# Performance work log

Hardware: AMD Instinct MI355X
Metric: run time of the kernel (lower is better)

The kernel has to match this reference:

```python
import jax, jax.numpy as jnp
import numpy as np

B, N, F, L = 4, 8192, 64, 2


def setup_inputs() -> dict:
    key = jax.random.key(0)
    k1, k2, k3 = jax.random.split(key, 3)
    x = jax.random.normal(k1, (B, N, F), dtype=jnp.float32)
    net_params = jax.random.normal(k2, (L * F * F,), dtype=jnp.float32)
    A = jax.random.normal(k3, (N, N), dtype=jnp.float32)
    return {"x": x, "t": 0, "net_params": net_params, "A": A}


def reference(x, t, net_params, A):
    # weights: [L, F, F]
    weights = net_params.reshape(L, F, F)
    # x: [B, N, F] (original does x.view(-1, A.size(1), features))
    z = x.reshape(-1, A.shape[1], F)
    for i in range(L):
        # GCN_operation: Z_out = A @ Z @ W_i  (the nested vmm loops emulate exactly this)
        h = jnp.einsum('mn,bnf->bmf', A, z)          # [B, N, F]
        z = jnp.einsum('bmf,fg->bmg', h, weights[i])  # [B, N, F]
        z = jax.nn.relu(z)
    return z
```

## Files before the change

kernel.cpp:

```cpp
#include <hip/hip_runtime.h>
#include <stdint.h>


#define MK 8192

typedef float f32x4 __attribute__((ext_vector_type(4)));
typedef uint32_t u32x4 __attribute__((ext_vector_type(4)));
typedef uint32_t u32x2 __attribute__((ext_vector_type(2)));
typedef __bf16 bf16x8 __attribute__((ext_vector_type(8)));

__device__ inline uint16_t f2bf(float f) {
  uint32_t u = __builtin_bit_cast(uint32_t, f);
  u += 0x7fffu + ((u >> 16) & 1u);
  return (uint16_t)(u >> 16);
}
__device__ inline float bf2f(uint32_t lo16) {
  return __builtin_bit_cast(float, lo16 << 16);
}

#define GLD(src, dstbase)                                                                    \
  __builtin_amdgcn_global_load_lds((const __attribute__((address_space(1))) uint32_t*)(src), \
                                   (__attribute__((address_space(3))) uint32_t*)(dstbase),   \
                                   16, 0, 0)

__global__ __launch_bounds__(256) void zw0(const float* __restrict__ x,
                                           const float* __restrict__ net,
                                           uint16_t* __restrict__ Zt) {
  __shared__ float Wl[64 * 64];
  __shared__ float rows[64][65];
  const int b = blockIdx.y, n0 = blockIdx.x * 64, tid = threadIdx.x;
  for (int i = tid * 4; i < 4096; i += 1024) {
    f32x4 v = *(const f32x4*)(net + i);
    Wl[i] = v[0]; Wl[i + 1] = v[1]; Wl[i + 2] = v[2]; Wl[i + 3] = v[3];
  }
  const float* src = x + ((uint64_t)b * MK + n0) * 64;
  for (int i = tid * 4; i < 4096; i += 1024) {
    f32x4 v = *(const f32x4*)(src + i);
    int r = i >> 6, f = i & 63;
    rows[r][f] = v[0]; rows[r][f + 1] = v[1]; rows[r][f + 2] = v[2]; rows[r][f + 3] = v[3];
  }
  __syncthreads();
  const int nl = tid & 63, g0 = (tid >> 6) * 16;
  float s[16];
#pragma unroll
  for (int j = 0; j < 16; ++j) s[j] = 0.f;
  for (int f = 0; f < 64; ++f) {
    float rv = rows[nl][f];
#pragma unroll
    for (int j = 0; j < 16; ++j) s[j] = fmaf(rv, Wl[f * 64 + g0 + j], s[j]);
  }
  uint16_t* dst = Zt + (uint64_t)(b * 64 + g0) * MK + n0 + nl;
#pragma unroll
  for (int j = 0; j < 16; ++j) dst[(uint64_t)j * MK] = f2bf(s[j]);
}

__global__ __launch_bounds__(512, 2) void gemm1(const float* __restrict__ Af,
                                                const uint16_t* __restrict__ Bt,
                                                uint16_t* __restrict__ Ab,
                                                uint16_t* __restrict__ P) {
  __shared__ __align__(16) uint16_t LB[65536];
#define AS1(b) (LB + (b)*16384)
#define BS1(b) (LB + 32768 + (b)*16384)
  const int bid = (int)blockIdx.x;
  const int s = bid & 7, bm = bid >> 3;
  const int row0 = bm * 256, k0 = s * 1024;
  const int tid = threadIdx.x, wid = tid >> 6, lane = tid & 63;
  const int wr = wid >> 2, wc = wid & 3;

  const int lsub = lane >> 3;
  const int ksrc = ((lane & 7) ^ lsub) << 3;
  const uint16_t* gB0 = Bt + (uint64_t)(4 * wid * 8 + lsub) * MK + k0 + ksrc;
  const int lBo = 4 * wid * 512;

  const int arow = (8 * wid) * 4 + (lane >> 4);
  const int acol = (lane & 15) * 4;
  const float* gA0 = Af + (uint64_t)(row0 + arow) * MK + k0 + acol;
  const int koct = (lane & 15) >> 1, krem = (lane & 1) * 4;

  f32x4 acc[8][4] = {};
  f32x4 rv[8];

  auto loadA = [&](int kofs) {
#pragma unroll
    for (int j = 0; j < 8; ++j)
      rv[j] = __builtin_nontemporal_load((const f32x4*)(gA0 + (uint64_t)j * 4 * MK + kofs));
  };
  auto stageA = [&](int buf, int kofs) {
#pragma unroll
    for (int j = 0; j < 8; ++j) {
      const int r = arow + j * 4;
      u32x2 w;
      w[0] = (uint32_t)f2bf(rv[j][0]) | ((uint32_t)f2bf(rv[j][1]) << 16);
      w[1] = (uint32_t)f2bf(rv[j][2]) | ((uint32_t)f2bf(rv[j][3]) << 16);
      *(u32x2*)&AS1(buf)[r * 64 + ((koct ^ (r & 7)) << 3) + krem] = w;
      *(u32x2*)(Ab + (uint64_t)(row0 + r) * MK + k0 + kofs + acol) = w;
    }
  };

  loadA(0);
#pragma unroll
  for (int j = 0; j < 4; ++j) GLD(gB0 + (uint64_t)j * 8 * MK, &BS1(0)[lBo + j * 512]);
  stageA(0, 0);
  __syncthreads();

  int buf = 0;
  for (int t = 0; t < 16; ++t) {
    const int nxt = (t + 1) * 64;
    if (t < 15) {
      loadA(nxt);
#pragma unroll
      for (int j = 0; j < 4; ++j) GLD(gB0 + (uint64_t)j * 8 * MK + nxt, &BS1(buf ^ 1)[lBo + j * 512]);
    }
#pragma unroll
    for (int kk = 0; kk < 2; ++kk) {
      const int kb = kk * 4 + (lane >> 4);
      bf16x8 a[8], b[4];
#pragma unroll
      for (int mi = 0; mi < 8; ++mi) {
        const int r = wr * 128 + mi * 16 + (lane & 15);
        a[mi] = *(const bf16x8*)&AS1(buf)[r * 64 + ((kb ^ (r & 7)) << 3)];
      }
#pragma unroll
      for (int n = 0; n < 4; ++n) {
        const int r = wc * 64 + n * 16 + (lane & 15);
        b[n] = *(const bf16x8*)&BS1(buf)[r * 64 + ((kb ^ (r & 7)) << 3)];
      }
#pragma unroll
      for (int mi = 0; mi < 8; ++mi)
#pragma unroll
        for (int n = 0; n < 4; ++n)
          acc[mi][n] = __builtin_amdgcn_mfma_f32_16x16x32_bf16(a[mi], b[n], acc[mi][n], 0, 0, 0);
    }
    if (t < 15) stageA(buf ^ 1, nxt);
    __syncthreads();
    buf ^= 1;
  }

  __syncthreads();
  const int lr = (lane >> 4) * 4, lc = lane & 15;
#pragma unroll
  for (int mi = 0; mi < 8; ++mi)
#pragma unroll
    for (int n = 0; n < 4; ++n)
#pragma unroll
      for (int j = 0; j < 4; ++j)
        LB[(wr * 128 + mi * 16 + lr + j) * 256 + (wc * 64 + n * 16 + lc)] = f2bf(acc[mi][n][j]);
  __syncthreads();
  uint16_t* Pp = P + (uint64_t)s * 2097152 + (uint64_t)row0 * 256;
#pragma unroll
  for (int i = 0; i < 16; ++i) {
    u32x4 v = *(const u32x4*)&LB[i * 4096 + tid * 8];
    *(u32x4*)(Pp + i * 4096 + tid * 8) = v;
  }
#undef AS1
#undef BS1
}

__global__ __launch_bounds__(512, 2) void gemm2(const uint16_t* __restrict__ Ab,
                                                const uint16_t* __restrict__ Bt,
                                                uint16_t* __restrict__ P) {
  __shared__ __align__(16) uint16_t LB[65536];
#define AS2(b) (LB + (b)*16384)
#define BS2(b) (LB + 32768 + (b)*16384)
  const int bid = (int)blockIdx.x;
  const int s = bid & 7, bm = bid >> 3;
  const int row0 = bm * 256, k0 = s * 1024;
  const int tid = threadIdx.x, wid = tid >> 6, lane = tid & 63;
  const int wr = wid >> 2, wc = wid & 3;

  const int lsub = lane >> 3;
  const int ksrc = ((lane & 7) ^ lsub) << 3;
  const uint16_t* gA0 = Ab + (uint64_t)(row0 + 4 * wid * 8 + lsub) * MK + k0 + ksrc;
  const uint16_t* gB0 = Bt + (uint64_t)(4 * wid * 8 + lsub) * MK + k0 + ksrc;
  const int lo = 4 * wid * 512;

  f32x4 acc[8][4] = {};

#pragma unroll
  for (int j = 0; j < 4; ++j) {
    GLD(gA0 + (uint64_t)j * 8 * MK, &AS2(0)[lo + j * 512]);
    GLD(gB0 + (uint64_t)j * 8 * MK, &BS2(0)[lo + j * 512]);
  }

  int buf = 0;
  for (int t = 0; t < 16; ++t) {
    const int tko = ((t + 1) < 16 ? (t + 1) : 15) * 64;
#pragma unroll
    for (int j = 0; j < 4; ++j) {
      GLD(gA0 + (uint64_t)j * 8 * MK + tko, &AS2(buf ^ 1)[lo + j * 512]);
      GLD(gB0 + (uint64_t)j * 8 * MK + tko, &BS2(buf ^ 1)[lo + j * 512]);
    }
    asm volatile("s_waitcnt vmcnt(8)" ::: "memory");
    __builtin_amdgcn_s_barrier();
    __builtin_amdgcn_sched_barrier(0);

    bf16x8 b[4][2];
#pragma unroll
    for (int n = 0; n < 4; ++n)
#pragma unroll
      for (int kk = 0; kk < 2; ++kk) {
        const int r = wc * 64 + n * 16 + (lane & 15);
        const int kb = kk * 4 + (lane >> 4);
        b[n][kk] = *(const bf16x8*)&BS2(buf)[r * 64 + ((kb ^ (r & 7)) << 3)];
      }
#pragma unroll
    for (int q = 0; q < 4; ++q) {
      bf16x8 a[2][2];
#pragma unroll
      for (int i = 0; i < 2; ++i)
#pragma unroll
        for (int kk = 0; kk < 2; ++kk) {
          const int r = wr * 128 + (2 * q + i) * 16 + (lane & 15);
          const int kb = kk * 4 + (lane >> 4);
          a[i][kk] = *(const bf16x8*)&AS2(buf)[r * 64 + ((kb ^ (r & 7)) << 3)];
        }
      __builtin_amdgcn_s_setprio(1);
#pragma unroll
      for (int kk = 0; kk < 2; ++kk)
#pragma unroll
        for (int i = 0; i < 2; ++i)
#pragma unroll
          for (int n = 0; n < 4; ++n)
            acc[2 * q + i][n] =
                __builtin_amdgcn_mfma_f32_16x16x32_bf16(a[i][kk], b[n][kk], acc[2 * q + i][n], 0, 0, 0);
      __builtin_amdgcn_s_setprio(0);
      __builtin_amdgcn_sched_barrier(0);
    }
    __builtin_amdgcn_s_barrier();
    buf ^= 1;
  }

  __syncthreads();
  const int lr = (lane >> 4) * 4, lc = lane & 15;
#pragma unroll
  for (int mi = 0; mi < 8; ++mi)
#pragma unroll
    for (int n = 0; n < 4; ++n)
#pragma unroll
      for (int j = 0; j < 4; ++j)
        LB[(wr * 128 + mi * 16 + lr + j) * 256 + (wc * 64 + n * 16 + lc)] = f2bf(acc[mi][n][j]);
  __syncthreads();
  uint16_t* Pp = P + (uint64_t)s * 2097152 + (uint64_t)row0 * 256;
#pragma unroll
  for (int i = 0; i < 16; ++i) {
    u32x4 v = *(const u32x4*)&LB[i * 4096 + tid * 8];
    *(u32x4*)(Pp + i * 4096 + tid * 8) = v;
  }
#undef AS2
#undef BS2
}

__global__ __launch_bounds__(256) void zw1P(const uint16_t* __restrict__ P,
                                            const float* __restrict__ net,
                                            uint16_t* __restrict__ Zt) {
  __shared__ float Wl[64 * 64];
  __shared__ float rows[64][65];
  const int b = blockIdx.y, n0 = blockIdx.x * 64, tid = threadIdx.x;
  const float* Wsrc = net + 4096;
  for (int i = tid * 4; i < 4096; i += 1024) {
    f32x4 v = *(const f32x4*)(Wsrc + i);
    Wl[i] = v[0]; Wl[i + 1] = v[1]; Wl[i + 2] = v[2]; Wl[i + 3] = v[3];
  }
#pragma unroll
  for (int g = 0; g < 2; ++g) {
    const int idx = (tid + g * 256) * 8;
    const int r = idx >> 6, f0 = idx & 63;
    const uint16_t* base = P + (uint64_t)(n0 + r) * 256 + b * 64 + f0;
    float acc8[8] = {};
#pragma unroll
    for (int sp = 0; sp < 8; ++sp) {
      u32x4 v = *(const u32x4*)(base + (uint64_t)sp * 2097152);
#pragma unroll
      for (int j = 0; j < 4; ++j) {
        acc8[2 * j]     += bf2f(v[j] & 0xffffu);
        acc8[2 * j + 1] += bf2f(v[j] >> 16);
      }
    }
#pragma unroll
    for (int j = 0; j < 8; ++j) rows[r][f0 + j] = fmaxf(acc8[j], 0.0f);
  }
  __syncthreads();
  const int nl = tid & 63, g0 = (tid >> 6) * 16;
  float s[16];
#pragma unroll
  for (int j = 0; j < 16; ++j) s[j] = 0.f;
  for (int f = 0; f < 64; ++f) {
    float rv = rows[nl][f];
#pragma unroll
    for (int j = 0; j < 16; ++j) s[j] = fmaf(rv, Wl[f * 64 + g0 + j], s[j]);
  }
  uint16_t* dst = Zt + (uint64_t)(b * 64 + g0) * MK + n0 + nl;
#pragma unroll
  for (int j = 0; j < 16; ++j) dst[(uint64_t)j * MK] = f2bf(s[j]);
}

__global__ __launch_bounds__(256) void combineF(const uint16_t* __restrict__ P,
                                                float* __restrict__ out) {
  const uint64_t e = ((uint64_t)blockIdx.x * 256 + threadIdx.x) * 8;
  float acc8[8] = {};
#pragma unroll
  for (int sp = 0; sp < 8; ++sp) {
    u32x4 v = *(const u32x4*)&P[(uint64_t)sp * 2097152 + e];
#pragma unroll
    for (int j = 0; j < 4; ++j) {
      acc8[2 * j]     += bf2f(v[j] & 0xffffu);
      acc8[2 * j + 1] += bf2f(v[j] >> 16);
    }
  }
  const int m = (int)(e >> 8);
  const int c = (int)(e & 255);
  float* dst = &out[(((uint64_t)(c >> 6)) * MK + m) * 64 + (c & 63)];
  f32x4 w0, w1;
#pragma unroll
  for (int j = 0; j < 4; ++j) { w0[j] = fmaxf(acc8[j], 0.0f); w1[j] = fmaxf(acc8[4 + j], 0.0f); }
  *(f32x4*)dst = w0;
  *(f32x4*)(dst + 4) = w1;
}

extern "C" void kernel_launch(void* const* d_in, const int* in_sizes, int n_in,
                              void* d_out, int out_size, void* d_ws, size_t ws_size,
                              hipStream_t stream) {
  const float* x   = (const float*)d_in[0];
  const float* net = (const float*)d_in[2];
  const float* A   = (const float*)d_in[3];
  float* out = (float*)d_out;

  uint16_t* Ab = (uint16_t*)d_ws;
  uint16_t* Zt = (uint16_t*)((char*)d_ws + 134217728ull);
  uint16_t* P  = (uint16_t*)((char*)d_ws + 142606336ull);

  zw0<<<dim3(128, 4), dim3(256), 0, stream>>>(x, net, Zt);
  gemm1<<<dim3(256), dim3(512), 0, stream>>>(A, Zt, Ab, P);
  zw1P<<<dim3(128, 4), dim3(256), 0, stream>>>(P, net, Zt);
  gemm2<<<dim3(256), dim3(512), 0, stream>>>(Ab, Zt, P);
  combineF<<<dim3(1024), dim3(256), 0, stream>>>(P, out);
}
```

Measured before the change: 167.7 us.

## Halve gemm1 K-tile to 32 to cut LDS and registers, split epilogue

Shrinks gemm1's per-stage K tile from 64 to 32, so double-buffered LDS drops from 128KB to 64KB. The A-staging is remapped so each thread converts one row segment with 16-byte stores, and B loads use new swizzle indices. The epilogue now writes the output through LDS in two halves, one per warp-row group, so it fits the smaller buffer. The aim is to allow more resident blocks and fewer A-staging registers, at the cost of twice as many barrier-separated iterations with less MFMA work between syncs.

```diff
diff --git a/kernel.cpp b/kernel.cpp
--- a/kernel.cpp
+++ b/kernel.cpp
@@ -58,99 +58,107 @@
                                                 const uint16_t* __restrict__ Bt,
                                                 uint16_t* __restrict__ Ab,
                                                 uint16_t* __restrict__ P) {
-  __shared__ __align__(16) uint16_t LB[65536];
-#define AS1(b) (LB + (b)*16384)
-#define BS1(b) (LB + 32768 + (b)*16384)
+  __shared__ __align__(16) uint16_t LB[32768];
+#define AS1(b) (LB + (b)*8192)
+#define BS1(b) (LB + 16384 + (b)*8192)
   const int bid = (int)blockIdx.x;
   const int s = bid & 7, bm = bid >> 3;
   const int row0 = bm * 256, k0 = s * 1024;
   const int tid = threadIdx.x, wid = tid >> 6, lane = tid & 63;
   const int wr = wid >> 2, wc = wid & 3;
 
-  const int lsub = lane >> 3;
-  const int ksrc = ((lane & 7) ^ lsub) << 3;
-  const uint16_t* gB0 = Bt + (uint64_t)(4 * wid * 8 + lsub) * MK + k0 + ksrc;
-  const int lBo = 4 * wid * 512;
-
-  const int arow = (8 * wid) * 4 + (lane >> 4);
-  const int acol = (lane & 15) * 4;
-  const float* gA0 = Af + (uint64_t)(row0 + arow) * MK + k0 + acol;
-  const int koct = (lane & 15) >> 1, krem = (lane & 1) * 4;
+  const int ar = tid >> 1, h = tid & 1;
+  const float* gA = Af + (uint64_t)(row0 + ar) * MK + k0 + h * 16;
+  uint16_t* AbW = Ab + (uint64_t)(row0 + ar) * MK + k0 + h * 16;
+
+  const int brow = lane >> 2, bpos = lane & 3, bsrc = bpos ^ (brow & 3);
+  const uint16_t* gBa = Bt + (uint64_t)((2 * wid) * 16 + brow) * MK + k0 + bsrc * 8;
+  const uint16_t* gBb = Bt + (uint64_t)((2 * wid + 1) * 16 + brow) * MK + k0 + bsrc * 8;
+  const int lBa = (2 * wid) * 512, lBb = (2 * wid + 1) * 512;
 
   f32x4 acc[8][4] = {};
-  f32x4 rv[8];
+  f32x4 rv[4];
 
   auto loadA = [&](int kofs) {
 #pragma unroll
-    for (int j = 0; j < 8; ++j)
-      rv[j] = __builtin_nontemporal_load((const f32x4*)(gA0 + (uint64_t)j * 4 * MK + kofs));
+    for (int j = 0; j < 4; ++j)
+      rv[j] = __builtin_nontemporal_load((const f32x4*)(gA + kofs + j * 4));
   };
   auto stageA = [&](int buf, int kofs) {
-#pragma unroll
-    for (int j = 0; j < 8; ++j) {
-      const int r = arow + j * 4;
-      u32x2 w;
-      w[0] = (uint32_t)f2bf(rv[j][0]) | ((uint32_t)f2bf(rv[j][1]) << 16);
-      w[1] = (uint32_t)f2bf(rv[j][2]) | ((uint32_t)f2bf(rv[j][3]) << 16);
-      *(u32x2*)&AS1(buf)[r * 64 + ((koct ^ (r & 7)) << 3) + krem] = w;
-      *(u32x2*)(Ab + (uint64_t)(row0 + r) * MK + k0 + kofs + acol) = w;
-    }
+    u32x4 w0, w1;
+    w0[0] = (uint32_t)f2bf(rv[0][0]) | ((uint32_t)f2bf(rv[0][1]) << 16);
+    w0[1] = (uint32_t)f2bf(rv[0][2]) | ((uint32_t)f2bf(rv[0][3]) << 16);
+    w0[2] = (uint32_t)f2bf(rv[1][0]) | ((uint32_t)f2bf(rv[1][1]) << 16);
+    w0[3] = (uint32_t)f2bf(rv[1][2]) | ((uint32_t)f2bf(rv[1][3]) << 16);
+    w1[0] = (uint32_t)f2bf(rv[2][0]) | ((uint32_t)f2bf(rv[2][1]) << 16);
+    w1[1] = (uint32_t)f2bf(rv[2][2]) | ((uint32_t)f2bf(rv[2][3]) << 16);
+    w1[2] = (uint32_t)f2bf(rv[3][0]) | ((uint32_t)f2bf(rv[3][1]) << 16);
+    w1[3] = (uint32_t)f2bf(rv[3][2]) | ((uint32_t)f2bf(rv[3][3]) << 16);
+    const int o0 = 2 * h, o1 = 2 * h + 1;
+    *(u32x4*)&AS1(buf)[ar * 32 + ((o0 ^ (ar & 3)) << 3)] = w0;
+    *(u32x4*)&AS1(buf)[ar * 32 + ((o1 ^ (ar & 3)) << 3)] = w1;
+    *(u32x4*)(AbW + kofs) = w0;
+    *(u32x4*)(AbW + kofs + 8) = w1;
   };
+  auto stageB = [&](int buf, int kofs) {
+    GLD(gBa + kofs, &BS1(buf)[lBa]);
+    GLD(gBb + kofs, &BS1(buf)[lBb]);
+  };
+  auto compute = [&](int buf) {
+    const int fr = lane & 15, fk = lane >> 4;
+    bf16x8 a[8], b[4];
+#pragma unroll
+    for (int mi = 0; mi < 8; ++mi) {
+      const int r = wr * 128 + mi * 16 + fr;
+      a[mi] = *(const bf16x8*)&AS1(buf)[r * 32 + ((fk ^ (r & 3)) << 3)];
+    }
+#pragma unroll
+    for (int n = 0; n < 4; ++n) {
+      const int r = wc * 64 + n * 16 + fr;
+      b[n] = *(const bf16x8*)&BS1(buf)[r * 32 + ((fk ^ (r & 3)) << 3)];
+    }
+#pragma unroll
+    for (int mi = 0; mi < 8; ++mi)
+#pragma unroll
+      for (int n = 0; n < 4; ++n)
+        acc[mi][n] = __builtin_amdgcn_mfma_f32_16x16x32_bf16(a[mi], b[n], acc[mi][n], 0, 0, 0);
+  };
 
   loadA(0);
-#pragma unroll
-  for (int j = 0; j < 4; ++j) GLD(gB0 + (uint64_t)j * 8 * MK, &BS1(0)[lBo + j * 512]);
+  stageB(0, 0);
   stageA(0, 0);
   __syncthreads();
 
   int buf = 0;
-  for (int t = 0; t < 16; ++t) {
-    const int nxt = (t + 1) * 64;
-    if (t < 15) {
-      loadA(nxt);
-#pragma unroll
-      for (int j = 0; j < 4; ++j) GLD(gB0 + (uint64_t)j * 8 * MK + nxt, &BS1(buf ^ 1)[lBo + j * 512]);
-    }
-#pragma unroll
-    for (int kk = 0; kk < 2; ++kk) {
-      const int kb = kk * 4 + (lane >> 4);
-      bf16x8 a[8], b[4];
-#pragma unroll
-      for (int mi = 0; mi < 8; ++mi) {
-        const int r = wr * 128 + mi * 16 + (lane & 15);
-        a[mi] = *(const bf16x8*)&AS1(buf)[r * 64 + ((kb ^ (r & 7)) << 3)];
-      }
-#pragma unroll
-      for (int n = 0; n < 4; ++n) {
-        const int r = wc * 64 + n * 16 + (lane & 15);
-        b[n] = *(const bf16x8*)&BS1(buf)[r * 64 + ((kb ^ (r & 7)) << 3)];
-      }
-#pragma unroll
-      for (int mi = 0; mi < 8; ++mi)
-#pragma unroll
-        for (int n = 0; n < 4; ++n)
-          acc[mi][n] = __builtin_amdgcn_mfma_f32_16x16x32_bf16(a[mi], b[n], acc[mi][n], 0, 0, 0);
-    }
-    if (t < 15) stageA(buf ^ 1, nxt);
+  for (int t = 0; t < 32; ++t) {
+    const int nxt = (t + 1) * 32;
+    if (t < 31) { loadA(nxt); stageB(buf ^ 1, nxt); }
+    compute(buf);
+    if (t < 31) stageA(buf ^ 1, nxt);
     __syncthreads();
     buf ^= 1;
   }
 
-  __syncthreads();
+  uint16_t* Pp = P + (uint64_t)s * 2097152 + (uint64_t)row0 * 256;
   const int lr = (lane >> 4) * 4, lc = lane & 15;
 #pragma unroll
-  for (int mi = 0; mi < 8; ++mi)
-#pragma unroll
-    for (int n = 0; n < 4; ++n)
-#pragma unroll
-      for (int j = 0; j < 4; ++j)
-        LB[(wr * 128 + mi * 16 + lr + j) * 256 + (wc * 64 + n * 16 + lc)] = f2bf(acc[mi][n][j]);
-  __syncthreads();
-  uint16_t* Pp = P + (uint64_t)s * 2097152 + (uint64_t)row0 * 256;
-#pragma unroll
-  for (int i = 0; i < 16; ++i) {
-    u32x4 v = *(const u32x4*)&LB[i * 4096 + tid * 8];
-    *(u32x4*)(Pp + i * 4096 + tid * 8) = v;
+  for (int half = 0; half < 2; ++half) {
+    __syncthreads();
+    if (wr == half) {
+#pragma unroll
+      for (int mi = 0; mi < 8; ++mi)
+#pragma unroll
+        for (int n = 0; n < 4; ++n)
+#pragma unroll
+          for (int j = 0; j < 4; ++j)
+            LB[(mi * 16 + lr + j) * 256 + (wc * 64 + n * 16 + lc)] = f2bf(acc[mi][n][j]);
+    }
+    __syncthreads();
+#pragma unroll
+    for (int i = 0; i < 8; ++i) {
+      u32x4 v = *(const u32x4*)&LB[i * 4096 + tid * 8];
+      *(u32x4*)(Pp + half * 32768 + i * 4096 + tid * 8) = v;
+    }
   }
 #undef AS1
 #undef BS1
```

Result: slower. 278.7 us (+66.1%).

## Store bf16 A in MFMA-fragment order and load A fragments directly to registers

Applied to the files above, without the earlier changes.

gemm1 now gives each wave a 32-row by 256-column tile, so each wave needs only its own A rows. It loads those rows straight from global memory into MFMA fragment registers and writes the bf16 copy of A in a per-wave, per-fragment chunked layout. gemm2 reads A fragments from that layout directly into registers with a ping-pong prefetch, and only B is staged through LDS. This drops A's LDS staging and the LDS traffic that goes with it, but each wave now reads all 256 columns of B from LDS, and A is loaded with plain global loads whose latency has less cover.

```diff
diff --git a/kernel.cpp b/kernel.cpp
--- a/kernel.cpp
+++ b/kernel.cpp
@@ -22,6 +22,7 @@
   __builtin_amdgcn_global_load_lds((const __attribute__((address_space(1))) uint32_t*)(src), \
                                    (__attribute__((address_space(3))) uint32_t*)(dstbase),   \
                                    16, 0, 0)
+#define CHOFF(t, w, mi, kk) ((uint64_t)((((t)*8 + (w)) * 2 + (mi)) * 2 + (kk)) * 512)
 
 __global__ __launch_bounds__(256) void zw0(const float* __restrict__ x,
                                            const float* __restrict__ net,
@@ -59,92 +60,94 @@
                                                 uint16_t* __restrict__ Ab,
                                                 uint16_t* __restrict__ P) {
   __shared__ __align__(16) uint16_t LB[65536];
-#define AS1(b) (LB + (b)*16384)
-#define BS1(b) (LB + 32768 + (b)*16384)
+#define BS1(b) (LB + (b)*16384)
   const int bid = (int)blockIdx.x;
   const int s = bid & 7, bm = bid >> 3;
   const int row0 = bm * 256, k0 = s * 1024;
   const int tid = threadIdx.x, wid = tid >> 6, lane = tid & 63;
-  const int wr = wid >> 2, wc = wid & 3;
+  const int fr = lane & 15, fk = lane >> 4;
 
   const int lsub = lane >> 3;
   const int ksrc = ((lane & 7) ^ lsub) << 3;
   const uint16_t* gB0 = Bt + (uint64_t)(4 * wid * 8 + lsub) * MK + k0 + ksrc;
   const int lBo = 4 * wid * 512;
 
-  const int arow = (8 * wid) * 4 + (lane >> 4);
-  const int acol = (lane & 15) * 4;
-  const float* gA0 = Af + (uint64_t)(row0 + arow) * MK + k0 + acol;
-  const int koct = (lane & 15) >> 1, krem = (lane & 1) * 4;
-
-  f32x4 acc[8][4] = {};
-  f32x4 rv[8];
-
-  auto loadA = [&](int kofs) {
-#pragma unroll
-    for (int j = 0; j < 8; ++j)
-      rv[j] = __builtin_nontemporal_load((const f32x4*)(gA0 + (uint64_t)j * 4 * MK + kofs));
+  const float* gA[2];
+#pragma unroll
+  for (int mi = 0; mi < 2; ++mi)
+    gA[mi] = Af + (uint64_t)(row0 + wid * 32 + mi * 16 + fr) * MK + k0 + fk * 8;
+  uint16_t* AbR = Ab + (uint64_t)(bm * 8 + s) * 262144 + lane * 8;
+
+  f32x4 acc[2][16] = {};
+  f32x4 rv[2][2][2];
+  bf16x8 a[2][2];
+
+  auto loadA = [&](int t) {
+#pragma unroll
+    for (int mi = 0; mi < 2; ++mi)
+#pragma unroll
+      for (int kk = 0; kk < 2; ++kk) {
+        rv[mi][kk][0] = __builtin_nontemporal_load((const f32x4*)(gA[mi] + t * 64 + kk * 32));
+        rv[mi][kk][1] = __builtin_nontemporal_load((const f32x4*)(gA[mi] + t * 64 + kk * 32 + 4));
+      }
   };
-  auto stageA = [&](int buf, int kofs) {
-#pragma unroll
-    for (int j = 0; j < 8; ++j) {
-      const int r = arow + j * 4;
-      u32x2 w;
-      w[0] = (uint32_t)f2bf(rv[j][0]) | ((uint32_t)f2bf(rv[j][1]) << 16);
-      w[1] = (uint32_t)f2bf(rv[j][2]) | ((uint32_t)f2bf(rv[j][3]) << 16);
-      *(u32x2*)&AS1(buf)[r * 64 + ((koct ^ (r & 7)) << 3) + krem] = w;
-      *(u32x2*)(Ab + (uint64_t)(row0 + r) * MK + k0 + kofs + acol) = w;
-    }
+  auto cvtStoreA = [&](int t) {
+#pragma unroll
+    for (int mi = 0; mi < 2; ++mi)
+#pragma unroll
+      for (int kk = 0; kk < 2; ++kk) {
+        u32x4 w;
+        w[0] = (uint32_t)f2bf(rv[mi][kk][0][0]) | ((uint32_t)f2bf(rv[mi][kk][0][1]) << 16);
+        w[1] = (uint32_t)f2bf(rv[mi][kk][0][2]) | ((uint32_t)f2bf(rv[mi][kk][0][3]) << 16);
+        w[2] = (uint32_t)f2bf(rv[mi][kk][1][0]) | ((uint32_t)f2bf(rv[mi][kk][1][1]) << 16);
+        w[3] = (uint32_t)f2bf(rv[mi][kk][1][2]) | ((uint32_t)f2bf(rv[mi][kk][1][3]) << 16);
+        a[mi][kk] = __builtin_bit_cast(bf16x8, w);
+        *(u32x4*)(AbR + CHOFF(t, wid, mi, kk)) = w;
+      }
   };
+  auto compute = [&](int buf) {
+    const uint16_t* B = BS1(buf);
+#pragma unroll
+    for (int n = 0; n < 16; ++n) {
+      const int r = n * 16 + fr, e = r & 7;
+      bf16x8 b0 = *(const bf16x8*)&B[r * 64 + ((fk ^ e) << 3)];
+      bf16x8 b1 = *(const bf16x8*)&B[r * 64 + (((4 + fk) ^ e) << 3)];
+#pragma unroll
+      for (int mi = 0; mi < 2; ++mi) {
+        acc[mi][n] = __builtin_amdgcn_mfma_f32_16x16x32_bf16(a[mi][0], b0, acc[mi][n], 0, 0, 0);
+        acc[mi][n] = __builtin_amdgcn_mfma_f32_16x16x32_bf16(a[mi][1], b1, acc[mi][n], 0, 0, 0);
+      }
+    }
+  };
 
   loadA(0);
 #pragma unroll
   for (int j = 0; j < 4; ++j) GLD(gB0 + (uint64_t)j * 8 * MK, &BS1(0)[lBo + j * 512]);
-  stageA(0, 0);
+  cvtStoreA(0);
   __syncthreads();
 
   int buf = 0;
   for (int t = 0; t < 16; ++t) {
-    const int nxt = (t + 1) * 64;
     if (t < 15) {
-      loadA(nxt);
+      loadA(t + 1);
+      const int nxt = (t + 1) * 64;
 #pragma unroll
       for (int j = 0; j < 4; ++j) GLD(gB0 + (uint64_t)j * 8 * MK + nxt, &BS1(buf ^ 1)[lBo + j * 512]);
     }
-#pragma unroll
-    for (int kk = 0; kk < 2; ++kk) {
-      const int kb = kk * 4 + (lane >> 4);
-      bf16x8 a[8], b[4];
-#pragma unroll
-      for (int mi = 0; mi < 8; ++mi) {
-        const int r = wr * 128 + mi * 16 + (lane & 15);
-        a[mi] = *(const bf16x8*)&AS1(buf)[r * 64 + ((kb ^ (r & 7)) << 3)];
-      }
-#pragma unroll
-      for (int n = 0; n < 4; ++n) {
-        const int r = wc * 64 + n * 16 + (lane & 15);
-        b[n] = *(const bf16x8*)&BS1(buf)[r * 64 + ((kb ^ (r & 7)) << 3)];
-      }
-#pragma unroll
-      for (int mi = 0; mi < 8; ++mi)
-#pragma unroll
-        for (int n = 0; n < 4; ++n)
-          acc[mi][n] = __builtin_amdgcn_mfma_f32_16x16x32_bf16(a[mi], b[n], acc[mi][n], 0, 0, 0);
-    }
-    if (t < 15) stageA(buf ^ 1, nxt);
+    compute(buf);
+    if (t < 15) cvtStoreA(t + 1);
     __syncthreads();
     buf ^= 1;
   }
 
-  __syncthreads();
-  const int lr = (lane >> 4) * 4, lc = lane & 15;
-#pragma unroll
-  for (int mi = 0; mi < 8; ++mi)
-#pragma unroll
-    for (int n = 0; n < 4; ++n)
+  const int lr = fk * 4, lc = fr;
+#pragma unroll
+  for (int mi = 0; mi < 2; ++mi)
+#pragma unroll
+    for (int n = 0; n < 16; ++n)
 #pragma unroll
       for (int j = 0; j < 4; ++j)
-        LB[(wr * 128 + mi * 16 + lr + j) * 256 + (wc * 64 + n * 16 + lc)] = f2bf(acc[mi][n][j]);
+        LB[(wid * 32 + mi * 16 + lr + j) * 256 + n * 16 + lc] = f2bf(acc[mi][n][j]);
   __syncthreads();
   uint16_t* Pp = P + (uint64_t)s * 2097152 + (uint64_t)row0 * 256;
 #pragma unroll
@@ -152,7 +155,6 @@
     u32x4 v = *(const u32x4*)&LB[i * 4096 + tid * 8];
     *(u32x4*)(Pp + i * 4096 + tid * 8) = v;
   }
-#undef AS1
 #undef BS1
 }
 
@@ -160,85 +162,83 @@
                                                 const uint16_t* __restrict__ Bt,
                                                 uint16_t* __restrict__ P) {
   __shared__ __align__(16) uint16_t LB[65536];
-#define AS2(b) (LB + (b)*16384)
-#define BS2(b) (LB + 32768 + (b)*16384)
+#define BS2(b) (LB + (b)*16384)
   const int bid = (int)blockIdx.x;
   const int s = bid & 7, bm = bid >> 3;
   const int row0 = bm * 256, k0 = s * 1024;
   const int tid = threadIdx.x, wid = tid >> 6, lane = tid & 63;
-  const int wr = wid >> 2, wc = wid & 3;
+  const int fr = lane & 15, fk = lane >> 4;
 
   const int lsub = lane >> 3;
   const int ksrc = ((lane & 7) ^ lsub) << 3;
-  const uint16_t* gA0 = Ab + (uint64_t)(row0 + 4 * wid * 8 + lsub) * MK + k0 + ksrc;
   const uint16_t* gB0 = Bt + (uint64_t)(4 * wid * 8 + lsub) * MK + k0 + ksrc;
-  const int lo = 4 * wid * 512;
-
-  f32x4 acc[8][4] = {};
-
-#pragma unroll
-  for (int j = 0; j < 4; ++j) {
-    GLD(gA0 + (uint64_t)j * 8 * MK, &AS2(0)[lo + j * 512]);
-    GLD(gB0 + (uint64_t)j * 8 * MK, &BS2(0)[lo + j * 512]);
-  }
-
-  int buf = 0;
-  for (int t = 0; t < 16; ++t) {
-    const int tko = ((t + 1) < 16 ? (t + 1) : 15) * 64;
-#pragma unroll
-    for (int j = 0; j < 4; ++j) {
-      GLD(gA0 + (uint64_t)j * 8 * MK + tko, &AS2(buf ^ 1)[lo + j * 512]);
-      GLD(gB0 + (uint64_t)j * 8 * MK + tko, &BS2(buf ^ 1)[lo + j * 512]);
-    }
-    asm volatile("s_waitcnt vmcnt(8)" ::: "memory");
-    __builtin_amdgcn_s_barrier();
-    __builtin_amdgcn_sched_barrier(0);
-
-    bf16x8 b[4][2];
-#pragma unroll
-    for (int n = 0; n < 4; ++n)
-#pragma unroll
-      for (int kk = 0; kk < 2; ++kk) {
-        const int r = wc * 64 + n * 16 + (lane & 15);
-        const int kb = kk * 4 + (lane >> 4);
-        b[n][kk] = *(const bf16x8*)&BS2(buf)[r * 64 + ((kb ^ (r & 7)) << 3)];
-      }
-#pragma unroll
-    for (int q = 0; q < 4; ++q) {
-      bf16x8 a[2][2];
-#pragma unroll
-      for (int i = 0; i < 2; ++i)
-#pragma unroll
-        for (int kk = 0; kk < 2; ++kk) {
-          const int r = wr * 128 + (2 * q + i) * 16 + (lane & 15);
-          const int kb = kk * 4 + (lane >> 4);
-          a[i][kk] = *(const bf16x8*)&AS2(buf)[r * 64 + ((kb ^ (r & 7)) << 3)];
-        }
-      __builtin_amdgcn_s_setprio(1);
-#pragma unroll
-      for (int kk = 0; kk < 2; ++kk)
-#pragma unroll
-        for (int i = 0; i < 2; ++i)
-#pragma unroll
-          for (int n = 0; n < 4; ++n)
-            acc[2 * q + i][n] =
-                __builtin_amdgcn_mfma_f32_16x16x32_bf16(a[i][kk], b[n][kk], acc[2 * q + i][n], 0, 0, 0);
-      __builtin_amdgcn_s_setprio(0);
-      __builtin_amdgcn_sched_barrier(0);
-    }
-    __builtin_amdgcn_s_barrier();
-    buf ^= 1;
-  }
-
-  __syncthreads();
-  const int lr = (lane >> 4) * 4, lc = lane & 15;
-#pragma unroll
-  for (int mi = 0; mi < 8; ++mi)
-#pragma unroll
-    for (int n = 0; n < 4; ++n)
+  const int lBo = 4 * wid * 512;
+  const uint16_t* AbR = Ab + (uint64_t)(bm * 8 + s) * 262144 + lane * 8;
+
+  f32x4 acc[2][16] = {};
+  bf16x8 aC[2][2], aN[2][2];
+
+  auto compute = [&](int buf, const bf16x8 (&a)[2][2]) {
+    const uint16_t* B = BS2(buf);
+#pragma unroll
+    for (int n = 0; n < 16; ++n) {
+      const int r = n * 16 + fr, e = r & 7;
+      bf16x8 b0 = *(const bf16x8*)&B[r * 64 + ((fk ^ e) << 3)];
+      bf16x8 b1 = *(const bf16x8*)&B[r * 64 + (((4 + fk) ^ e) << 3)];
+#pragma unroll
+      for (int mi = 0; mi < 2; ++mi) {
+        acc[mi][n] = __builtin_amdgcn_mfma_f32_16x16x32_bf16(a[mi][0], b0, acc[mi][n], 0, 0, 0);
+        acc[mi][n] = __builtin_amdgcn_mfma_f32_16x16x32_bf16(a[mi][1], b1, acc[mi][n], 0, 0, 0);
+      }
+    }
+  };
+
+#pragma unroll
+  for (int mi = 0; mi < 2; ++mi)
+#pragma unroll
+    for (int kk = 0; kk < 2; ++kk)
+      aC[mi][kk] = *(const bf16x8*)(AbR + CHOFF(0, wid, mi, kk));
+#pragma unroll
+  for (int j = 0; j < 4; ++j) GLD(gB0 + (uint64_t)j * 8 * MK, &BS2(0)[lBo + j * 512]);
+  __syncthreads();
+
+  for (int tt = 0; tt < 16; tt += 2) {
+    {
+      const int nxt = (tt + 1) * 64;
+#pragma unroll
+      for (int j = 0; j < 4; ++j) GLD(gB0 + (uint64_t)j * 8 * MK + nxt, &BS2(1)[lBo + j * 512]);
+#pragma unroll
+      for (int mi = 0; mi < 2; ++mi)
+#pragma unroll
+        for (int kk = 0; kk < 2; ++kk)
+          aN[mi][kk] = *(const bf16x8*)(AbR + CHOFF(tt + 1, wid, mi, kk));
+      compute(0, aC);
+      __syncthreads();
+    }
+    {
+      if (tt + 2 < 16) {
+        const int nxt = (tt + 2) * 64;
+#pragma unroll
+        for (int j = 0; j < 4; ++j) GLD(gB0 + (uint64_t)j * 8 * MK + nxt, &BS2(0)[lBo + j * 512]);
+#pragma unroll
+        for (int mi = 0; mi < 2; ++mi)
+#pragma unroll
+          for (int kk = 0; kk < 2; ++kk)
+            aC[mi][kk] = *(const bf16x8*)(AbR + CHOFF(tt + 2, wid, mi, kk));
+      }
+      compute(1, aN);
+      __syncthreads();
+    }
+  }
+
+  const int lr = fk * 4, lc = fr;
+#pragma unroll
+  for (int mi = 0; mi < 2; ++mi)
+#pragma unroll
+    for (int n = 0; n < 16; ++n)
 #pragma unroll
       for (int j = 0; j < 4; ++j)
-        LB[(wr * 128 + mi * 16 + lr + j) * 256 + (wc * 64 + n * 16 + lc)] = f2bf(acc[mi][n][j]);
+        LB[(wid * 32 + mi * 16 + lr + j) * 256 + n * 16 + lc] = f2bf(acc[mi][n][j]);
   __syncthreads();
   uint16_t* Pp = P + (uint64_t)s * 2097152 + (uint64_t)row0 * 256;
 #pragma unroll
@@ -246,7 +246,6 @@
     u32x4 v = *(const u32x4*)&LB[i * 4096 + tid * 8];
     *(u32x4*)(Pp + i * 4096 + tid * 8) = v;
   }
-#undef AS2
 #undef BS2
 }
 
```

Result: slower. 184.2 us (+9.8%).
